# Optimization experiments

Hardware: AMD Instinct MI355X
Metric: run time of the kernel (lower is better)

Reference implementation:

```python
import jax, jax.numpy as jnp
import numpy as np

N, E, G, F_IN, D = 50000, 400000, 256, 79, 400
BN_EPS = 1e-5


def setup_inputs() -> dict:
    key = jax.random.key(0)
    ks = jax.random.split(key, 16)
    w = lambda k, s: jax.random.normal(k, s, dtype=jnp.float32) * 0.05
    return {
        "x": jax.random.normal(ks[0], (N, F_IN), dtype=jnp.float32),
        "edge_index": jax.random.randint(ks[1], (2, E), 0, N, dtype=jnp.int32),
        "batch_index": jnp.sort(jax.random.randint(ks[2], (N,), 0, G, dtype=jnp.int32)),
        "num_graphs": G,
        "mlp1_w1": w(ks[3], (F_IN, D)), "mlp1_b1": jnp.zeros(D, jnp.float32),
        "mlp1_bn_g": jnp.ones(D, jnp.float32), "mlp1_bn_b": jnp.zeros(D, jnp.float32),
        "mlp1_bn_m": jnp.zeros(D, jnp.float32), "mlp1_bn_v": jnp.ones(D, jnp.float32),
        "mlp1_w2": w(ks[4], (D, D)), "mlp1_b2": jnp.zeros(D, jnp.float32),
        "mlp2_w1": w(ks[5], (D, D)), "mlp2_b1": jnp.zeros(D, jnp.float32),
        "mlp2_bn_g": jnp.ones(D, jnp.float32), "mlp2_bn_b": jnp.zeros(D, jnp.float32),
        "mlp2_bn_m": jnp.zeros(D, jnp.float32), "mlp2_bn_v": jnp.ones(D, jnp.float32),
        "mlp2_w2": w(ks[6], (D, D)), "mlp2_b2": jnp.zeros(D, jnp.float32),
        "out1_w": w(ks[7], (D, D)), "out1_b": jnp.zeros(D, jnp.float32),
        "out2_w": w(ks[8], (D, D)), "out2_b": jnp.zeros(D, jnp.float32),
        "out3_w": w(ks[9], (D, D)), "out3_b": jnp.zeros(D, jnp.float32),
        "out_w": w(ks[10], (2 * D, 1)), "out_b": jnp.zeros(1, jnp.float32),
        "eps1": jnp.full((1,), 5e-5, jnp.float32),
        "eps2": jnp.full((1,), 5e-5, jnp.float32),
        "eps3": jnp.full((1,), 5e-5, jnp.float32),
    }


def _bn(z, g, b, m, v):
    # BatchNorm1d in inference mode (running stats)
    return (z - m) * jax.lax.rsqrt(v + BN_EPS) * g + b


def _gin(h, src, dst, eps, w1, b1, g, bb, m, v, w2, b2):
    n = h.shape[0]
    agg = jax.ops.segment_sum(h[src], dst, num_segments=n)  # [N, d] scatter-add
    z = (1.0 + eps) * h + agg
    z = jax.nn.relu(_bn(z @ w1 + b1, g, bb, m, v))
    return jax.nn.relu(z @ w2 + b2)


def reference(x, edge_index, batch_index, num_graphs,
              mlp1_w1, mlp1_b1, mlp1_bn_g, mlp1_bn_b, mlp1_bn_m, mlp1_bn_v, mlp1_w2, mlp1_b2,
              mlp2_w1, mlp2_b1, mlp2_bn_g, mlp2_bn_b, mlp2_bn_m, mlp2_bn_v, mlp2_w2, mlp2_b2,
              out1_w, out1_b, out2_w, out2_b, out3_w, out3_b, out_w, out_b,
              eps1, eps2, eps3):
    src, dst = edge_index[0], edge_index[1]
    h = _gin(x, src, dst, eps1[0], mlp1_w1, mlp1_b1, mlp1_bn_g, mlp1_bn_b, mlp1_bn_m, mlp1_bn_v, mlp1_w2, mlp1_b2)
    h = jnp.tanh(h @ out1_w + out1_b)
    h = _gin(h, src, dst, eps2[0], mlp2_w1, mlp2_b1, mlp2_bn_g, mlp2_bn_b, mlp2_bn_m, mlp2_bn_v, mlp2_w2, mlp2_b2)
    h = jnp.tanh(h @ out2_w + out2_b)
    h = _gin(h, src, dst, eps3[0], mlp2_w1, mlp2_b1, mlp2_bn_g, mlp2_bn_b, mlp2_bn_m, mlp2_bn_v, mlp2_w2, mlp2_b2)
    h = jnp.tanh(h @ out3_w + out3_b)
    # dropout is identity in eval mode
    mx = jax.ops.segment_max(h, batch_index, num_segments=num_graphs)   # global_max_pool
    sm = jax.ops.segment_sum(h, batch_index, num_segments=num_graphs)
    cnt = jax.ops.segment_sum(jnp.ones((h.shape[0], 1), h.dtype), batch_index, num_segments=num_graphs)
    mn = sm / jnp.maximum(cnt, 1.0)                                      # global_mean_pool
    pooled = jnp.concatenate([mx, mn], axis=1)                           # [G, 2D]
    return pooled @ out_w + out_b
```

## Files before the change

### kernel.cpp

```cpp
#include <hip/hip_runtime.h>
#include <math.h>

#define NN 50000
#define NE 400000
#define NG 256
#define FIN 79
#define DD 400
#define LDK 448
#define LDK1 128
#define XP 80
#define NPAD 512
#define BK 64
#define MT ((NN + 127) / 128)
#define BN_EPS_F 1e-5f

#define SCAN_B 256
#define SCAN_NB ((NN + SCAN_B - 1) / SCAN_B)

typedef unsigned short u16;
typedef unsigned short ushort8 __attribute__((ext_vector_type(8)));
typedef unsigned short ushort4v __attribute__((ext_vector_type(4)));
typedef short short8 __attribute__((ext_vector_type(8)));
typedef float floatx4 __attribute__((ext_vector_type(4)));

__device__ inline u16 f2bf(float f) {
    unsigned int u = __builtin_bit_cast(unsigned int, f);
    u += 0x7fffu + ((u >> 16) & 1u);
    return (u16)(u >> 16);
}
__device__ inline float bf2f(u16 s) {
    unsigned int u = ((unsigned int)s) << 16;
    return __builtin_bit_cast(float, u);
}
__device__ inline float fast_tanh(float x) {
    float e = __expf(2.0f * x);
    return 1.0f - 2.0f / (e + 1.0f);
}

__global__ void k_gstart(const int* __restrict__ batch, int* __restrict__ gstart) {
    int g = blockIdx.x * blockDim.x + threadIdx.x;
    if (g > NG) return;
    int lo = 0, hi = NN;
    while (lo < hi) {
        int mid = (lo + hi) >> 1;
        if (batch[mid] < g) lo = mid + 1; else hi = mid;
    }
    gstart[g] = lo;
}

__global__ void k_zero_int(int* __restrict__ p, int n) {
    int i = blockIdx.x * blockDim.x + threadIdx.x;
    if (i < n) p[i] = 0;
}
__global__ void k_hist(const int* __restrict__ dst, int* __restrict__ deg) {
    int e = blockIdx.x * blockDim.x + threadIdx.x;
    if (e < NE) atomicAdd(&deg[dst[e]], 1);
}

__global__ void k_scan_a(const int* __restrict__ deg, int* __restrict__ bsum) {
    __shared__ int red[SCAN_B];
    int i = blockIdx.x * SCAN_B + threadIdx.x;
    red[threadIdx.x] = (i < NN) ? deg[i] : 0;
    __syncthreads();
    for (int s = SCAN_B / 2; s > 0; s >>= 1) {
        if (threadIdx.x < s) red[threadIdx.x] += red[threadIdx.x + s];
        __syncthreads();
    }
    if (threadIdx.x == 0) bsum[blockIdx.x] = red[0];
}
__global__ void k_scan_b(const int* __restrict__ bsum, int* __restrict__ boff) {
    __shared__ int buf[SCAN_B];
    int t = threadIdx.x;
    int v = (t < SCAN_NB) ? bsum[t] : 0;
    buf[t] = v;
    __syncthreads();
    for (int off = 1; off < SCAN_B; off <<= 1) {
        int add = (t >= off) ? buf[t - off] : 0;
        __syncthreads();
        buf[t] += add;
        __syncthreads();
    }
    if (t < SCAN_NB) boff[t] = buf[t] - v;
}
__global__ void k_scan_c(const int* __restrict__ deg, const int* __restrict__ boff,
                         int* __restrict__ rowptr, int* __restrict__ cursor) {
    __shared__ int buf[SCAN_B];
    int b = blockIdx.x;
    int i = b * SCAN_B + threadIdx.x;
    int v = (i < NN) ? deg[i] : 0;
    buf[threadIdx.x] = v;
    __syncthreads();
    for (int off = 1; off < SCAN_B; off <<= 1) {
        int add = (threadIdx.x >= off) ? buf[threadIdx.x - off] : 0;
        __syncthreads();
        buf[threadIdx.x] += add;
        __syncthreads();
    }
    int excl = boff[b] + buf[threadIdx.x] - v;
    if (i < NN) { rowptr[i] = excl; cursor[i] = excl; }
    if (b == 0 && threadIdx.x == 0) rowptr[NN] = NE;
}

__global__ void k_fill(const int* __restrict__ src, const int* __restrict__ dst,
                       int* __restrict__ cursor, int* __restrict__ eidx) {
    int e = blockIdx.x * blockDim.x + threadIdx.x;
    if (e < NE) {
        int pos = atomicAdd(&cursor[dst[e]], 1);
        eidx[pos] = src[e];
    }
}

__global__ void k_packw(const float* __restrict__ W, int K, u16* __restrict__ Wt, int ldk) {
    int idx = blockIdx.x * 256 + threadIdx.x;
    int total = NPAD * ldk;
    if (idx >= total) return;
    int n = idx / ldk, k = idx - n * ldk;
    float v = (n < DD && k < K) ? W[(size_t)k * DD + n] : 0.0f;
    Wt[idx] = f2bf(v);
}

__global__ __launch_bounds__(256)
void k_packx(const float* __restrict__ x, u16* __restrict__ xb) {
    int idx = blockIdx.x * 256 + threadIdx.x;
    if (idx >= NN * XP) return;
    int n = idx / XP, c = idx - n * XP;
    xb[idx] = (c < FIN) ? f2bf(x[(size_t)n * FIN + c]) : (u16)0;
}

__global__ __launch_bounds__(256)
void k_agg1(const u16* __restrict__ xb, const int* __restrict__ rowptr,
            const int* __restrict__ eidx, const float* __restrict__ eps,
            u16* __restrict__ z0) {
    int wave = threadIdx.x >> 6, lane = threadIdx.x & 63;
    int n = blockIdx.x * 4 + wave;
    if (lane >= 32) return;
    u16* zr = z0 + (size_t)n * LDK1;
    if (lane >= 20) {
        ushort4v zz = {0, 0, 0, 0};
        *(ushort4v*)&zr[XP + (lane - 20) * 4] = zz;
        return;
    }
    float s = 1.0f + eps[0];
    int c4 = lane * 4;
    ushort4v v = *(const ushort4v*)&xb[(size_t)n * XP + c4];
    float a[4];
    #pragma unroll
    for (int t = 0; t < 4; ++t) a[t] = s * bf2f(v[t]);
    int e0 = rowptr[n], e1 = rowptr[n + 1];
    int i = e0;
    for (; i + 2 <= e1; i += 2) {
        int s0 = eidx[i], s1 = eidx[i + 1];
        ushort4v v0 = *(const ushort4v*)&xb[(size_t)s0 * XP + c4];
        ushort4v v1 = *(const ushort4v*)&xb[(size_t)s1 * XP + c4];
        #pragma unroll
        for (int t = 0; t < 4; ++t) a[t] += bf2f(v0[t]) + bf2f(v1[t]);
    }
    if (i < e1) {
        int s0 = eidx[i];
        ushort4v v0 = *(const ushort4v*)&xb[(size_t)s0 * XP + c4];
        #pragma unroll
        for (int t = 0; t < 4; ++t) a[t] += bf2f(v0[t]);
    }
    ushort4v o;
    #pragma unroll
    for (int t = 0; t < 4; ++t) o[t] = f2bf(a[t]);
    *(ushort4v*)&zr[c4] = o;
}

__global__ __launch_bounds__(256)
void k_agg(const u16* __restrict__ h, const int* __restrict__ rowptr,
           const int* __restrict__ eidx, const float* __restrict__ eps,
           u16* __restrict__ z) {
    int wave = threadIdx.x >> 6, lane = threadIdx.x & 63;
    int n = blockIdx.x * 4 + wave;
    if (lane >= 50) return;
    float s = 1.0f + eps[0];
    int c8 = lane * 8;
    ushort8 v = *(const ushort8*)(h + (size_t)n * LDK + c8);
    float a[8];
    #pragma unroll
    for (int t = 0; t < 8; ++t) a[t] = s * bf2f(v[t]);
    int e0 = rowptr[n], e1 = rowptr[n + 1];
    int i = e0;
    for (; i + 2 <= e1; i += 2) {
        int s0 = eidx[i], s1 = eidx[i + 1];
        ushort8 v0 = *(const ushort8*)(h + (size_t)s0 * LDK + c8);
        ushort8 v1 = *(const ushort8*)(h + (size_t)s1 * LDK + c8);
        #pragma unroll
        for (int t = 0; t < 8; ++t) a[t] += bf2f(v0[t]) + bf2f(v1[t]);
    }
    if (i < e1) {
        int s0 = eidx[i];
        ushort8 v0 = *(const ushort8*)(h + (size_t)s0 * LDK + c8);
        #pragma unroll
        for (int t = 0; t < 8; ++t) a[t] += bf2f(v0[t]);
    }
    ushort8 o;
    #pragma unroll
    for (int t = 0; t < 8; ++t) o[t] = f2bf(a[t]);
    *(ushort8*)(z + (size_t)n * LDK + c8) = o;
}

#define CSTR 136
__global__ __launch_bounds__(256, 3)
void k_gemm(const u16* __restrict__ A, int lda, int ktiles,
            const u16* __restrict__ Wt,
            const float* __restrict__ bias,
            const float* __restrict__ bng, const float* __restrict__ bnb,
            const float* __restrict__ bnm, const float* __restrict__ bnv,
            u16* __restrict__ Y, int mode)
{
    __shared__ u16 smem[128 * CSTR];
    u16* As = smem;
    u16* Bs = smem + 128 * BK;
    u16* Cs = smem;

    int id = blockIdx.x;
    int mt = (id >> 5) * 8 + (id & 7);
    int nt = (id & 31) >> 3;
    if (mt >= MT) return;
    int m0 = mt * 128;
    int n0 = nt * 128;

    int tid = threadIdx.x;
    int wave = tid >> 6, lane = tid & 63;
    int wm = wave & 1, wn = wave >> 1;

    int srow = lane >> 3;
    int sc   = lane & 7;
    int swz  = (sc ^ srow) << 3;
    int lm = lane & 15;
    int q  = lane >> 4;

    bool nactive = (n0 + wn * 64) < LDK;

    const u16* gA[4]; const u16* gB[4];
    int lofs[4];
    #pragma unroll
    for (int j = 0; j < 4; ++j) {
        int rowL = wave * 32 + j * 8 + srow;
        lofs[j] = rowL * BK + swz;
        int gr = m0 + rowL; gr = gr < NN ? gr : NN - 1;
        gA[j] = A + (size_t)gr * lda + sc * 8;
        gB[j] = Wt + (size_t)(n0 + rowL) * lda + sc * 8;
    }

    ushort8 va[4], vb[4];
    #pragma unroll
    for (int j = 0; j < 4; ++j) { va[j] = *(const ushort8*)gA[j]; vb[j] = *(const ushort8*)gB[j]; }

    floatx4 acc[4][4] = {};

    for (int kt = 0; kt < ktiles; ++kt) {
        __syncthreads();
        #pragma unroll
        for (int j = 0; j < 4; ++j) {
            *(ushort8*)&As[lofs[j]] = va[j];
            *(ushort8*)&Bs[lofs[j]] = vb[j];
        }
        __syncthreads();
        if (kt + 1 < ktiles) {
            int ko = (kt + 1) * BK;
            #pragma unroll
            for (int j = 0; j < 4; ++j) {
                va[j] = *(const ushort8*)(gA[j] + ko);
                vb[j] = *(const ushort8*)(gB[j] + ko);
            }
        }
        if (nactive) {
            #pragma unroll
            for (int ks = 0; ks < 2; ++ks) {
                short8 af[4], bf[4];
                #pragma unroll
                for (int i = 0; i < 4; ++i) {
                    int r = wm * 64 + i * 16 + lm;
                    int ch = (ks * 4 + q) ^ (lm & 7);
                    af[i] = *(const short8*)&As[r * BK + ch * 8];
                }
                #pragma unroll
                for (int j = 0; j < 4; ++j) {
                    int r = wn * 64 + j * 16 + lm;
                    int ch = (ks * 4 + q) ^ (lm & 7);
                    bf[j] = *(const short8*)&Bs[r * BK + ch * 8];
                }
                #pragma unroll
                for (int i = 0; i < 4; ++i)
                    #pragma unroll
                    for (int j = 0; j < 4; ++j)
                        acc[i][j] = __builtin_amdgcn_mfma_f32_16x16x32_bf16(af[i], bf[j], acc[i][j], 0, 0, 0);
            }
        }
    }
    __syncthreads();

    #pragma unroll
    for (int j = 0; j < 4; ++j) {
        int nl = wn * 64 + j * 16 + lm;
        int n  = n0 + nl;
        bool live = n < DD;
        float bias_c = 0.0f, sc2 = 1.0f, sh = 0.0f;
        if (live) {
            bias_c = bias[n];
            if (mode == 0) {
                sc2 = bng[n] * rsqrtf(bnv[n] + BN_EPS_F);
                sh = bnb[n] - bnm[n] * sc2;
            }
        }
        #pragma unroll
        for (int i = 0; i < 4; ++i) {
            int rl = wm * 64 + i * 16 + q * 4;
            #pragma unroll
            for (int r = 0; r < 4; ++r) {
                u16 o = 0;
                if (live) {
                    float val = acc[i][j][r] + bias_c;
                    if (mode == 0)      val = fmaxf(fmaf(val, sc2, sh), 0.0f);
                    else if (mode == 1) val = fmaxf(val, 0.0f);
                    else                val = fast_tanh(val);
                    o = f2bf(val);
                }
                if (nactive) Cs[(rl + r) * CSTR + nl] = o;
            }
        }
    }
    __syncthreads();

    int row = tid >> 1, half = tid & 1;
    int m = m0 + row;
    if (m < NN) {
        #pragma unroll
        for (int k = 0; k < 8; ++k) {
            int coloff = half * 64 + k * 8;
            int n = n0 + coloff;
            if (n < LDK) {
                ushort8 v = *(const ushort8*)&Cs[row * CSTR + coloff];
                *(ushort8*)&Y[(size_t)m * LDK + n] = v;
            }
        }
    }
}

__global__ __launch_bounds__(256)
void k_pool(const u16* __restrict__ t3, const int* __restrict__ gstart,
            float* __restrict__ pooled) {
    __shared__ float smax[4][408];
    __shared__ float ssum[4][408];
    int g = blockIdx.x;
    int wave = threadIdx.x >> 6, lane = threadIdx.x & 63;
    int s = gstart[g], e = gstart[g + 1];
    if (lane < 50) {
        int c8 = lane * 8;
        float mx[8], sm[8];
        #pragma unroll
        for (int t = 0; t < 8; ++t) { mx[t] = -INFINITY; sm[t] = 0.0f; }
        for (int n = s + wave; n < e; n += 4) {
            ushort8 v = *(const ushort8*)&t3[(size_t)n * LDK + c8];
            #pragma unroll
            for (int t = 0; t < 8; ++t) {
                float f = bf2f(v[t]);
                mx[t] = fmaxf(mx[t], f);
                sm[t] += f;
            }
        }
        #pragma unroll
        for (int t = 0; t < 8; ++t) {
            smax[wave][c8 + t] = mx[t];
            ssum[wave][c8 + t] = sm[t];
        }
    }
    __syncthreads();
    float cnt = fmaxf((float)(e - s), 1.0f);
    for (int c = threadIdx.x; c < DD; c += 256) {
        float m = fmaxf(fmaxf(smax[0][c], smax[1][c]), fmaxf(smax[2][c], smax[3][c]));
        float su = ssum[0][c] + ssum[1][c] + ssum[2][c] + ssum[3][c];
        pooled[(size_t)g * 2 * DD + c] = m;
        pooled[(size_t)g * 2 * DD + DD + c] = su / cnt;
    }
}

__global__ void k_final(const float* __restrict__ pooled, const float* __restrict__ w,
                        const float* __restrict__ b, float* __restrict__ out) {
    __shared__ float red[256];
    int g = blockIdx.x;
    float p = 0.0f;
    for (int j = threadIdx.x; j < 2 * DD; j += blockDim.x)
        p += pooled[(size_t)g * 2 * DD + j] * w[j];
    red[threadIdx.x] = p;
    __syncthreads();
    for (int s = 128; s > 0; s >>= 1) {
        if (threadIdx.x < s) red[threadIdx.x] += red[threadIdx.x + s];
        __syncthreads();
    }
    if (threadIdx.x == 0) out[g] = red[0] + b[0];
}

extern "C" void kernel_launch(void* const* d_in, const int* in_sizes, int n_in,
                              void* d_out, int out_size, void* d_ws, size_t ws_size,
                              hipStream_t stream) {
    const float* x     = (const float*)d_in[0];
    const int*   ei    = (const int*)d_in[1];
    const int*   batch = (const int*)d_in[2];
    const float* m1w1  = (const float*)d_in[4];
    const float* m1b1  = (const float*)d_in[5];
    const float* m1g   = (const float*)d_in[6];
    const float* m1bb  = (const float*)d_in[7];
    const float* m1m   = (const float*)d_in[8];
    const float* m1v   = (const float*)d_in[9];
    const float* m1w2  = (const float*)d_in[10];
    const float* m1b2  = (const float*)d_in[11];
    const float* m2w1  = (const float*)d_in[12];
    const float* m2b1  = (const float*)d_in[13];
    const float* m2g   = (const float*)d_in[14];
    const float* m2bb  = (const float*)d_in[15];
    const float* m2m   = (const float*)d_in[16];
    const float* m2v   = (const float*)d_in[17];
    const float* m2w2  = (const float*)d_in[18];
    const float* m2b2  = (const float*)d_in[19];
    const float* o1w   = (const float*)d_in[20];
    const float* o1b   = (const float*)d_in[21];
    const float* o2w   = (const float*)d_in[22];
    const float* o2b   = (const float*)d_in[23];
    const float* o3w   = (const float*)d_in[24];
    const float* o3b   = (const float*)d_in[25];
    const float* ow    = (const float*)d_in[26];
    const float* ob    = (const float*)d_in[27];
    const float* eps1  = (const float*)d_in[28];
    const float* eps2  = (const float*)d_in[29];
    const float* eps3  = (const float*)d_in[30];
    const int* srcI = ei;
    const int* dstI = ei + NE;

    u16* buf1 = (u16*)d_ws;
    u16* buf2 = buf1 + (size_t)NN * LDK;
    u16* buf3 = buf2 + (size_t)NN * LDK;
    u16* z0   = buf3 + (size_t)NN * LDK;
    u16* w1t  = z0 + (size_t)NN * LDK1;
    u16* m1w2t = w1t + (size_t)NPAD * LDK1;
    u16* m2w1t = m1w2t + (size_t)NPAD * LDK;
    u16* m2w2t = m2w1t + (size_t)NPAD * LDK;
    u16* o1t   = m2w2t + (size_t)NPAD * LDK;
    u16* o2t   = o1t + (size_t)NPAD * LDK;
    u16* o3t   = o2t + (size_t)NPAD * LDK;
    u16* xb    = o3t + (size_t)NPAD * LDK;
    float* pooled = (float*)(xb + (size_t)NN * XP);
    int* gstart = (int*)(pooled + (size_t)NG * 2 * DD);
    int* rowptr = gstart + (NG + 2);
    int* cursor = rowptr + (NN + 1);
    int* deg    = cursor + NN;
    int* eidx   = deg + NN;
    int* bsum   = eidx + NE;
    int* boff   = bsum + SCAN_NB;

    float* out = (float*)d_out;

    int gemmBlocks = ((MT + 7) / 8) * 32;

    k_gstart<<<2, 256, 0, stream>>>(batch, gstart);
    k_zero_int<<<(NN + 255) / 256, 256, 0, stream>>>(deg, NN);
    k_hist<<<(NE + 255) / 256, 256, 0, stream>>>(dstI, deg);
    k_scan_a<<<SCAN_NB, SCAN_B, 0, stream>>>(deg, bsum);
    k_scan_b<<<1, SCAN_B, 0, stream>>>(bsum, boff);
    k_scan_c<<<SCAN_NB, SCAN_B, 0, stream>>>(deg, boff, rowptr, cursor);
    k_fill<<<(NE + 255) / 256, 256, 0, stream>>>(srcI, dstI, cursor, eidx);

    int pw1 = (NPAD * LDK1 + 255) / 256;
    int pw = (NPAD * LDK + 255) / 256;
    k_packw<<<pw1, 256, 0, stream>>>(m1w1, FIN, w1t, LDK1);
    k_packw<<<pw, 256, 0, stream>>>(m1w2, DD, m1w2t, LDK);
    k_packw<<<pw, 256, 0, stream>>>(m2w1, DD, m2w1t, LDK);
    k_packw<<<pw, 256, 0, stream>>>(m2w2, DD, m2w2t, LDK);
    k_packw<<<pw, 256, 0, stream>>>(o1w, DD, o1t, LDK);
    k_packw<<<pw, 256, 0, stream>>>(o2w, DD, o2t, LDK);
    k_packw<<<pw, 256, 0, stream>>>(o3w, DD, o3t, LDK);
    k_packx<<<(NN * XP + 255) / 256, 256, 0, stream>>>(x, xb);

    k_agg1<<<NN / 4, 256, 0, stream>>>(xb, rowptr, eidx, eps1, z0);
    k_gemm<<<gemmBlocks, 256, 0, stream>>>(z0, LDK1, LDK1 / BK, w1t, m1b1,
                                           m1g, m1bb, m1m, m1v, buf1, 0);
    k_gemm<<<gemmBlocks, 256, 0, stream>>>(buf1, LDK, LDK / BK, m1w2t, m1b2,
                                           nullptr, nullptr, nullptr, nullptr, buf2, 1);
    k_gemm<<<gemmBlocks, 256, 0, stream>>>(buf2, LDK, LDK / BK, o1t, o1b,
                                           nullptr, nullptr, nullptr, nullptr, buf3, 2);

    k_agg<<<NN / 4, 256, 0, stream>>>(buf3, rowptr, eidx, eps2, buf1);
    k_gemm<<<gemmBlocks, 256, 0, stream>>>(buf1, LDK, LDK / BK, m2w1t, m2b1,
                                           m2g, m2bb, m2m, m2v, buf2, 0);
    k_gemm<<<gemmBlocks, 256, 0, stream>>>(buf2, LDK, LDK / BK, m2w2t, m2b2,
                                           nullptr, nullptr, nullptr, nullptr, buf1, 1);
    k_gemm<<<gemmBlocks, 256, 0, stream>>>(buf1, LDK, LDK / BK, o2t, o2b,
                                           nullptr, nullptr, nullptr, nullptr, buf2, 2);

    k_agg<<<NN / 4, 256, 0, stream>>>(buf2, rowptr, eidx, eps3, buf1);
    k_gemm<<<gemmBlocks, 256, 0, stream>>>(buf1, LDK, LDK / BK, m2w1t, m2b1,
                                           m2g, m2bb, m2m, m2v, buf3, 0);
    k_gemm<<<gemmBlocks, 256, 0, stream>>>(buf3, LDK, LDK / BK, m2w2t, m2b2,
                                           nullptr, nullptr, nullptr, nullptr, buf1, 1);
    k_gemm<<<gemmBlocks, 256, 0, stream>>>(buf1, LDK, LDK / BK, o3t, o3b,
                                           nullptr, nullptr, nullptr, nullptr, buf3, 2);

    k_pool<<<NG, 256, 0, stream>>>(buf3, gstart, pooled);
    k_final<<<NG, 256, 0, stream>>>(pooled, ow, ob, out);
}
```

Before: 876.1 us.

## Use direct global-to-LDS loads in GEMM, batch weight packing, unroll aggregation

```diff
diff --git a/kernel.cpp b/kernel.cpp
--- a/kernel.cpp
+++ b/kernel.cpp
@@ -37,6 +37,13 @@
     return 1.0f - 2.0f / (e + 1.0f);
 }
 
+__device__ __forceinline__ void gld_lds16(const u16* g, u16* l) {
+    __builtin_amdgcn_global_load_lds(
+        (const __attribute__((address_space(1))) unsigned int*)(size_t)(g),
+        (__attribute__((address_space(3))) unsigned int*)(unsigned int)(size_t)(l),
+        16, 0, 0);
+}
+
 __global__ void k_gstart(const int* __restrict__ batch, int* __restrict__ gstart) {
     int g = blockIdx.x * blockDim.x + threadIdx.x;
     if (g > NG) return;
@@ -110,10 +117,27 @@
     }
 }
 
-__global__ void k_packw(const float* __restrict__ W, int K, u16* __restrict__ Wt, int ldk) {
+__global__ __launch_bounds__(256)
+void k_packw_all(const float* __restrict__ w0, const float* __restrict__ w1,
+                 const float* __restrict__ w2, const float* __restrict__ w3,
+                 const float* __restrict__ w4, const float* __restrict__ w5,
+                 const float* __restrict__ w6,
+                 u16* __restrict__ d0, u16* __restrict__ d1, u16* __restrict__ d2,
+                 u16* __restrict__ d3, u16* __restrict__ d4, u16* __restrict__ d5,
+                 u16* __restrict__ d6) {
+    int which = blockIdx.y;
+    const float* W; u16* Wt; int ldk = LDK, K = DD;
+    switch (which) {
+        case 0: W = w0; Wt = d0; ldk = LDK1; K = FIN; break;
+        case 1: W = w1; Wt = d1; break;
+        case 2: W = w2; Wt = d2; break;
+        case 3: W = w3; Wt = d3; break;
+        case 4: W = w4; Wt = d4; break;
+        case 5: W = w5; Wt = d5; break;
+        default: W = w6; Wt = d6; break;
+    }
     int idx = blockIdx.x * 256 + threadIdx.x;
-    int total = NPAD * ldk;
-    if (idx >= total) return;
+    if (idx >= NPAD * ldk) return;
     int n = idx / ldk, k = idx - n * ldk;
     float v = (n < DD && k < K) ? W[(size_t)k * DD + n] : 0.0f;
     Wt[idx] = f2bf(v);
@@ -182,14 +206,17 @@
     for (int t = 0; t < 8; ++t) a[t] = s * bf2f(v[t]);
     int e0 = rowptr[n], e1 = rowptr[n + 1];
     int i = e0;
-    for (; i + 2 <= e1; i += 2) {
-        int s0 = eidx[i], s1 = eidx[i + 1];
+    for (; i + 4 <= e1; i += 4) {
+        int s0 = eidx[i], s1 = eidx[i + 1], s2 = eidx[i + 2], s3 = eidx[i + 3];
         ushort8 v0 = *(const ushort8*)(h + (size_t)s0 * LDK + c8);
         ushort8 v1 = *(const ushort8*)(h + (size_t)s1 * LDK + c8);
-        #pragma unroll
-        for (int t = 0; t < 8; ++t) a[t] += bf2f(v0[t]) + bf2f(v1[t]);
-    }
-    if (i < e1) {
+        ushort8 v2 = *(const ushort8*)(h + (size_t)s2 * LDK + c8);
+        ushort8 v3 = *(const ushort8*)(h + (size_t)s3 * LDK + c8);
+        #pragma unroll
+        for (int t = 0; t < 8; ++t)
+            a[t] += (bf2f(v0[t]) + bf2f(v1[t])) + (bf2f(v2[t]) + bf2f(v3[t]));
+    }
+    for (; i < e1; ++i) {
         int s0 = eidx[i];
         ushort8 v0 = *(const ushort8*)(h + (size_t)s0 * LDK + c8);
         #pragma unroll
@@ -202,7 +229,7 @@
 }
 
 #define CSTR 136
-__global__ __launch_bounds__(256, 3)
+__global__ __launch_bounds__(256, 4)
 void k_gemm(const u16* __restrict__ A, int lda, int ktiles,
             const u16* __restrict__ Wt,
             const float* __restrict__ bias,
@@ -228,45 +255,27 @@
 
     int srow = lane >> 3;
     int sc   = lane & 7;
-    int swz  = (sc ^ srow) << 3;
     int lm = lane & 15;
     int q  = lane >> 4;
 
     bool nactive = (n0 + wn * 64) < LDK;
 
-    const u16* gA[4]; const u16* gB[4];
-    int lofs[4];
-    #pragma unroll
-    for (int j = 0; j < 4; ++j) {
-        int rowL = wave * 32 + j * 8 + srow;
-        lofs[j] = rowL * BK + swz;
-        int gr = m0 + rowL; gr = gr < NN ? gr : NN - 1;
-        gA[j] = A + (size_t)gr * lda + sc * 8;
-        gB[j] = Wt + (size_t)(n0 + rowL) * lda + sc * 8;
-    }
-
-    ushort8 va[4], vb[4];
-    #pragma unroll
-    for (int j = 0; j < 4; ++j) { va[j] = *(const ushort8*)gA[j]; vb[j] = *(const ushort8*)gB[j]; }
-
     floatx4 acc[4][4] = {};
 
     for (int kt = 0; kt < ktiles; ++kt) {
-        __syncthreads();
+        int k0 = kt * BK;
         #pragma unroll
         for (int j = 0; j < 4; ++j) {
-            *(ushort8*)&As[lofs[j]] = va[j];
-            *(ushort8*)&Bs[lofs[j]] = vb[j];
-        }
-        __syncthreads();
-        if (kt + 1 < ktiles) {
-            int ko = (kt + 1) * BK;
-            #pragma unroll
-            for (int j = 0; j < 4; ++j) {
-                va[j] = *(const ushort8*)(gA[j] + ko);
-                vb[j] = *(const ushort8*)(gB[j] + ko);
-            }
-        }
+            int row = wave * 32 + j * 8 + srow;
+            int cs = sc ^ (row & 7);
+            int gr = m0 + row; gr = gr < NN ? gr : NN - 1;
+            gld_lds16(A + (size_t)gr * lda + k0 + (cs << 3),
+                      &As[(wave * 32 + j * 8) * BK]);
+            gld_lds16(Wt + (size_t)(n0 + row) * lda + k0 + (cs << 3),
+                      &Bs[(wave * 32 + j * 8) * BK]);
+        }
+        __syncthreads();
+
         if (nactive) {
             #pragma unroll
             for (int ks = 0; ks < 2; ++ks) {
@@ -274,13 +283,13 @@
                 #pragma unroll
                 for (int i = 0; i < 4; ++i) {
                     int r = wm * 64 + i * 16 + lm;
-                    int ch = (ks * 4 + q) ^ (lm & 7);
+                    int ch = (ks * 4 + q) ^ (r & 7);
                     af[i] = *(const short8*)&As[r * BK + ch * 8];
                 }
                 #pragma unroll
                 for (int j = 0; j < 4; ++j) {
                     int r = wn * 64 + j * 16 + lm;
-                    int ch = (ks * 4 + q) ^ (lm & 7);
+                    int ch = (ks * 4 + q) ^ (r & 7);
                     bf[j] = *(const short8*)&Bs[r * BK + ch * 8];
                 }
                 #pragma unroll
@@ -290,8 +299,8 @@
                         acc[i][j] = __builtin_amdgcn_mfma_f32_16x16x32_bf16(af[i], bf[j], acc[i][j], 0, 0, 0);
             }
         }
-    }
-    __syncthreads();
+        __syncthreads();
+    }
 
     #pragma unroll
     for (int j = 0; j < 4; ++j) {
@@ -319,7 +328,7 @@
                     else                val = fast_tanh(val);
                     o = f2bf(val);
                 }
-                if (nactive) Cs[(rl + r) * CSTR + nl] = o;
+                Cs[(rl + r) * CSTR + nl] = o;
             }
         }
     }
@@ -463,15 +472,9 @@
     k_scan_c<<<SCAN_NB, SCAN_B, 0, stream>>>(deg, boff, rowptr, cursor);
     k_fill<<<(NE + 255) / 256, 256, 0, stream>>>(srcI, dstI, cursor, eidx);
 
-    int pw1 = (NPAD * LDK1 + 255) / 256;
-    int pw = (NPAD * LDK + 255) / 256;
-    k_packw<<<pw1, 256, 0, stream>>>(m1w1, FIN, w1t, LDK1);
-    k_packw<<<pw, 256, 0, stream>>>(m1w2, DD, m1w2t, LDK);
-    k_packw<<<pw, 256, 0, stream>>>(m2w1, DD, m2w1t, LDK);
-    k_packw<<<pw, 256, 0, stream>>>(m2w2, DD, m2w2t, LDK);
-    k_packw<<<pw, 256, 0, stream>>>(o1w, DD, o1t, LDK);
-    k_packw<<<pw, 256, 0, stream>>>(o2w, DD, o2t, LDK);
-    k_packw<<<pw, 256, 0, stream>>>(o3w, DD, o3t, LDK);
+    dim3 pwGrid((NPAD * LDK + 255) / 256, 7);
+    k_packw_all<<<pwGrid, 256, 0, stream>>>(m1w1, m1w2, m2w1, m2w2, o1w, o2w, o3w,
+                                            w1t, m1w2t, m2w1t, m2w2t, o1t, o2t, o3t);
     k_packx<<<(NN * XP + 255) / 256, 256, 0, stream>>>(x, xb);
 
     k_agg1<<<NN / 4, 256, 0, stream>>>(xb, rowptr, eidx, eps1, z0);
```

Measured after the change: 806.1 us. 8.0% less time.
